# Performance work log

Measured on AMD Instinct MI355X. Metric: run time of the kernel, lower is better.

## Reference

```python
import jax, jax.numpy as jnp
import numpy as np

N_NODES = 50000
DIM_IN = 256
DIM_OUT = 256
N_EDGES = 1600000


def setup_inputs() -> dict:
    key = jax.random.key(0)
    k1, k2, k3, k4, k5 = jax.random.split(key, 5)
    feature = jax.random.normal(k1, (N_NODES, DIM_IN), dtype=jnp.float32)
    src = jax.random.randint(k2, (N_EDGES,), 0, N_NODES, dtype=jnp.int32)
    dst = jax.random.randint(k3, (N_EDGES,), 0, N_NODES, dtype=jnp.int32)
    # Linear(dim_in, dim_out) params
    bound = 1.0 / np.sqrt(DIM_IN)
    W = jax.random.uniform(k4, (DIM_OUT, DIM_IN), dtype=jnp.float32, minval=-bound, maxval=bound)
    b = jax.random.uniform(k5, (DIM_OUT,), dtype=jnp.float32, minval=-bound, maxval=bound)
    return {"feature": feature, "src": src, "dst": dst, "W": W, "b": b}


def reference(feature, src, dst, W, b):
    # copy_u: gather source features per edge; mean-reduce per destination node.
    msg_sum = jax.ops.segment_sum(feature[src], dst, num_segments=N_NODES)  # [N, Din]
    deg = jax.ops.segment_sum(jnp.ones((src.shape[0],), feature.dtype), dst,
                              num_segments=N_NODES)  # [N]
    mean = msg_sum / jnp.maximum(deg, 1.0)[:, None]
    # DGL update_all only overwrites 'h' for nodes that received messages;
    # isolated (in-degree 0) nodes keep their original feature.
    h = jnp.where((deg > 0)[:, None], mean, feature)
    # apply_nodes: Linear on all nodes
    return h @ W.T + b
```

## Files before the change

kernel.cpp:

```cpp
#include <hip/hip_runtime.h>
#include <hip/hip_bf16.h>

#define N_NODES 50000
#define NPAD 50016
#define DUMMY 50000
#define DIM 256
#define N_EDGES 1600000
#define NBUK 196
#define CAP 10240
#define CHUNK_E 4096
#define NBLK ((N_EDGES + CHUNK_E - 1) / CHUNK_E)
#define GEMM_BLKS ((N_NODES + 63) / 64)
#define NCHUNK 8
#define AGG_BPC 782
#define NGROUP (N_NODES / 16)
#define LROW 72

typedef float f32x4 __attribute__((ext_vector_type(4)));
typedef __bf16 bf16x8 __attribute__((ext_vector_type(8)));
typedef __bf16 bf16x4 __attribute__((ext_vector_type(4)));
typedef unsigned long long u64;
typedef unsigned int u32;
typedef unsigned short u16;

__global__ __launch_bounds__(256) void setup_k(const float* __restrict__ W,
                                               __bf16* __restrict__ Wbf,
                                               int* __restrict__ bcur,
                                               __bf16* __restrict__ Yc) {
    int i = blockIdx.x * 256 + threadIdx.x;
    Wbf[i] = (__bf16)W[i];
    if (i < NBUK) bcur[i] = i * CAP;
    if (i < NCHUNK * (NPAD - N_NODES) * 32) {
        int c = i >> 9;
        int rem = i & 511;
        Yc[(size_t)c * NPAD * 32 + (size_t)(N_NODES + (rem >> 5)) * 32 + (rem & 31)] = (__bf16)0.0f;
    }
}

__global__ __launch_bounds__(256) void fused_k(const float* __restrict__ feat,
                                               const __bf16* __restrict__ Wbf,
                                               __bf16* __restrict__ Yc,
                                               const int* __restrict__ src,
                                               const int* __restrict__ dst,
                                               int* __restrict__ bcur,
                                               unsigned int* __restrict__ staged) {
    __shared__ __bf16 lw[256 * LROW];
    __shared__ int lh[NBUK];
    __shared__ int lbase[NBUK];

    if (blockIdx.x < GEMM_BLKS) {
        const int wid  = threadIdx.x >> 6;
        const int lane = threadIdx.x & 63;
        const int row0 = blockIdx.x * 64 + wid * 16;
        const int mrow = lane & 15;
        const int kgrp = lane >> 4;

        int arow = row0 + mrow;
        int arow_c = arow < N_NODES ? arow : (N_NODES - 1);
        const float* aptr = feat + (size_t)arow_c * DIM + kgrp * 8;

        const int t = threadIdx.x;
        const int srow = t >> 3;
        const int scb  = (t & 7) * 8;

        f32x4 acc[16];
#pragma unroll
        for (int i = 0; i < 16; ++i) acc[i] = (f32x4)0.0f;

        for (int p = 0; p < 4; ++p) {
            f32x4 ar0 = *(const f32x4*)(aptr + (p * 2) * 32);
            f32x4 ar1 = *(const f32x4*)(aptr + (p * 2) * 32 + 4);
            f32x4 ar2 = *(const f32x4*)(aptr + (p * 2 + 1) * 32);
            f32x4 ar3 = *(const f32x4*)(aptr + (p * 2 + 1) * 32 + 4);

            if (p) __syncthreads();
#pragma unroll
            for (int i = 0; i < 8; ++i) {
                int row = srow + i * 32;
                uint4 v = *(const uint4*)(Wbf + (size_t)row * DIM + p * 64 + scb);
                *(uint4*)(lw + row * LROW + scb) = v;
            }
            __syncthreads();

            bf16x8 af0, af1;
            af0[0] = (__bf16)ar0[0]; af0[1] = (__bf16)ar0[1];
            af0[2] = (__bf16)ar0[2]; af0[3] = (__bf16)ar0[3];
            af0[4] = (__bf16)ar1[0]; af0[5] = (__bf16)ar1[1];
            af0[6] = (__bf16)ar1[2]; af0[7] = (__bf16)ar1[3];
            af1[0] = (__bf16)ar2[0]; af1[1] = (__bf16)ar2[1];
            af1[2] = (__bf16)ar2[2]; af1[3] = (__bf16)ar2[3];
            af1[4] = (__bf16)ar3[0]; af1[5] = (__bf16)ar3[1];
            af1[6] = (__bf16)ar3[2]; af1[7] = (__bf16)ar3[3];

#pragma unroll
            for (int nt = 0; nt < 16; ++nt) {
                const __bf16* lp = lw + (nt * 16 + mrow) * LROW + kgrp * 8;
                bf16x8 wf0 = *(const bf16x8*)(lp);
                bf16x8 wf1 = *(const bf16x8*)(lp + 32);
                acc[nt] = __builtin_amdgcn_mfma_f32_16x16x32_bf16(wf0, af0, acc[nt], 0, 0, 0);
                acc[nt] = __builtin_amdgcn_mfma_f32_16x16x32_bf16(wf1, af1, acc[nt], 0, 0, 0);
            }
        }

        const int node = row0 + mrow;
        if (node < N_NODES) {
#pragma unroll
            for (int nt = 0; nt < 16; ++nt) {
                int oc0 = nt * 16 + kgrp * 4;
                bf16x4 pv;
                pv[0] = (__bf16)acc[nt][0];
                pv[1] = (__bf16)acc[nt][1];
                pv[2] = (__bf16)acc[nt][2];
                pv[3] = (__bf16)acc[nt][3];
                __bf16* yp = Yc + (size_t)(oc0 >> 5) * NPAD * 32
                                + (size_t)node * 32 + (oc0 & 31);
                *(bf16x4*)yp = pv;
            }
        }
    } else {
        int pb = blockIdx.x - GEMM_BLKS;
        for (int i = threadIdx.x; i < NBUK; i += 256) lh[i] = 0;
        __syncthreads();
        int base = pb * CHUNK_E;
        int end = base + CHUNK_E; if (end > N_EDGES) end = N_EDGES;
        for (int e = base + threadIdx.x; e < end; e += 256)
            atomicAdd(&lh[dst[e] >> 8], 1);
        __syncthreads();
        for (int i = threadIdx.x; i < NBUK; i += 256) {
            int c = lh[i];
            lbase[i] = c ? atomicAdd(&bcur[i], c) : 0;
            lh[i] = 0;
        }
        __syncthreads();
        for (int e = base + threadIdx.x; e < end; e += 256) {
            int d = dst[e];
            int s = src[e];
            int b = d >> 8;
            int p = atomicAdd(&lh[b], 1);
            staged[lbase[b] + p] = (unsigned int)s | ((unsigned int)(d & 255) << 16);
        }
    }
}

__global__ __launch_bounds__(256) void finalize_k(const unsigned int* __restrict__ staged,
                                                  const int* __restrict__ bcur,
                                                  int* __restrict__ offs,
                                                  u16* __restrict__ deg16,
                                                  u16* __restrict__ edge16) {
    __shared__ int nh[256];
    __shared__ int nbase[256];
    __shared__ int sm[256];
    int t = threadIdx.x, b = blockIdx.x;
    int beg = b * CAP;
    int cnt = bcur[b] - beg;
    nh[t] = 0;
    __syncthreads();
    for (int i = t; i < cnt; i += 256)
        atomicAdd(&nh[staged[beg + i] >> 16], 1);
    __syncthreads();
    int v = nh[t];
    int v8 = (v + 7) & ~7;
    sm[t] = v8;
    __syncthreads();
    for (int off = 1; off < 256; off <<= 1) {
        int x = (t >= off) ? sm[t - off] : 0;
        __syncthreads();
        sm[t] += x;
        __syncthreads();
    }
    nbase[t] = sm[t] - v8;
    int node = (b << 8) + t;
    if (node < N_NODES) {
        offs[node]  = beg + nbase[t];
        deg16[node] = (u16)v;
    }
    for (int i = v; i < v8; ++i)
        edge16[beg + nbase[t] + i] = (u16)DUMMY;
    nh[t] = 0;
    __syncthreads();
    for (int i = t; i < cnt; i += 256) {
        unsigned int u = staged[beg + i];
        int dl = (int)(u >> 16);
        int p = atomicAdd(&nh[dl], 1);
        edge16[beg + nbase[dl] + p] = (u16)(u & 0xFFFFu);
    }
}

#define GQ(ev) (*(const uint4*)(Ybase + (size_t)((u32)(ev) & 0xffffu) * 32 + cl))
#define ACCQ(q) do { \
    a0 += __uint_as_float((q).x << 16); a1 += __uint_as_float((q).x); \
    a2 += __uint_as_float((q).y << 16); a3 += __uint_as_float((q).y); \
    a4 += __uint_as_float((q).z << 16); a5 += __uint_as_float((q).z); \
    a6 += __uint_as_float((q).w << 16); a7 += __uint_as_float((q).w); \
} while (0)

__global__ __launch_bounds__(256) void aggregate_k(const __bf16* __restrict__ Yc,
                                                   const int* __restrict__ offs,
                                                   const u16* __restrict__ deg16,
                                                   const u16* __restrict__ edge16,
                                                   const float* __restrict__ bias,
                                                   float* __restrict__ out) {
    const int chunk = blockIdx.x & 7;
    const int bic   = blockIdx.x >> 3;
    const int wid   = threadIdx.x >> 6;
    const int lane  = threadIdx.x & 63;
    const int seg   = lane >> 2;
    const int cl    = (lane & 3) * 8;

    const int g = bic * 4 + wid;
    if (g >= NGROUP) return;
    const int node = g * 16 + seg;

    const __bf16* Ybase = Yc + (size_t)chunk * NPAD * 32;
    const float* bp = bias + chunk * 32 + cl;
    const f32x4 bv0 = *(const f32x4*)bp;
    const f32x4 bv1 = *(const f32x4*)(bp + 4);

    const int beg = offs[node];
    const int dg  = (int)deg16[node];

    float a0 = 0.f, a1 = 0.f, a2 = 0.f, a3 = 0.f;
    float a4 = 0.f, a5 = 0.f, a6 = 0.f, a7 = 0.f;

    f32x4 r0, r1;
    if (dg > 0) {
        const int nb8 = (dg + 7) >> 3;
        const int npair = nb8 >> 1;
        const int odd = nb8 & 1;
        int j = beg;
        u64 eA = *(const u64*)(edge16 + j);
        u64 eB = *(const u64*)(edge16 + j + 4);
        u64 eC = *(const u64*)(edge16 + j + 8);
        u64 eD = *(const u64*)(edge16 + j + 12);
        for (int p = 0; p < npair; ++p) {
            u64 nA = *(const u64*)(edge16 + j + 16);
            u64 nB = *(const u64*)(edge16 + j + 20);
            u64 nC = *(const u64*)(edge16 + j + 24);
            u64 nD = *(const u64*)(edge16 + j + 28);
            uint4 q0 = GQ(eA);       uint4 q1 = GQ(eA >> 16);
            uint4 q2 = GQ(eA >> 32); uint4 q3 = GQ(eA >> 48);
            uint4 q4 = GQ(eB);       uint4 q5 = GQ(eB >> 16);
            uint4 q6 = GQ(eB >> 32); uint4 q7 = GQ(eB >> 48);
            uint4 q8 = GQ(eC);       uint4 q9 = GQ(eC >> 16);
            uint4 qa = GQ(eC >> 32); uint4 qb = GQ(eC >> 48);
            uint4 qc = GQ(eD);       uint4 qd = GQ(eD >> 16);
            uint4 qe = GQ(eD >> 32); uint4 qf = GQ(eD >> 48);
            ACCQ(q0); ACCQ(q1); ACCQ(q2); ACCQ(q3);
            ACCQ(q4); ACCQ(q5); ACCQ(q6); ACCQ(q7);
            ACCQ(q8); ACCQ(q9); ACCQ(qa); ACCQ(qb);
            ACCQ(qc); ACCQ(qd); ACCQ(qe); ACCQ(qf);
            j += 16;
            eA = nA; eB = nB; eC = nC; eD = nD;
        }
        if (odd) {
            uint4 q0 = GQ(eA);       uint4 q1 = GQ(eA >> 16);
            uint4 q2 = GQ(eA >> 32); uint4 q3 = GQ(eA >> 48);
            uint4 q4 = GQ(eB);       uint4 q5 = GQ(eB >> 16);
            uint4 q6 = GQ(eB >> 32); uint4 q7 = GQ(eB >> 48);
            ACCQ(q0); ACCQ(q1); ACCQ(q2); ACCQ(q3);
            ACCQ(q4); ACCQ(q5); ACCQ(q6); ACCQ(q7);
        }
        float inv = 1.0f / (float)dg;
        r0[0] = a0 * inv + bv0[0];
        r0[1] = a1 * inv + bv0[1];
        r0[2] = a2 * inv + bv0[2];
        r0[3] = a3 * inv + bv0[3];
        r1[0] = a4 * inv + bv1[0];
        r1[1] = a5 * inv + bv1[1];
        r1[2] = a6 * inv + bv1[2];
        r1[3] = a7 * inv + bv1[3];
    } else {
        uint4 q = *(const uint4*)(Ybase + (size_t)node * 32 + cl);
        r0[0] = __uint_as_float(q.x << 16) + bv0[0];
        r0[1] = __uint_as_float(q.x & 0xffff0000u) + bv0[1];
        r0[2] = __uint_as_float(q.y << 16) + bv0[2];
        r0[3] = __uint_as_float(q.y & 0xffff0000u) + bv0[3];
        r1[0] = __uint_as_float(q.z << 16) + bv1[0];
        r1[1] = __uint_as_float(q.z & 0xffff0000u) + bv1[1];
        r1[2] = __uint_as_float(q.w << 16) + bv1[2];
        r1[3] = __uint_as_float(q.w & 0xffff0000u) + bv1[3];
    }
    float* op = out + (size_t)node * DIM + chunk * 32 + cl;
    *(f32x4*)op = r0;
    *(f32x4*)(op + 4) = r1;
}

static inline size_t align64(size_t x) { return (x + 63) & ~(size_t)63; }

extern "C" void kernel_launch(void* const* d_in, const int* in_sizes, int n_in,
                              void* d_out, int out_size, void* d_ws, size_t ws_size,
                              hipStream_t stream) {
    const float* feature = (const float*)d_in[0];
    const int*   src     = (const int*)d_in[1];
    const int*   dst     = (const int*)d_in[2];
    const float* W       = (const float*)d_in[3];
    const float* b       = (const float*)d_in[4];
    float* out = (float*)d_out;

    char* ws = (char*)d_ws;
    __bf16* Yc  = (__bf16*)ws;               ws += align64((size_t)NCHUNK * NPAD * 32 * 2);
    __bf16* Wbf = (__bf16*)ws;               ws += align64((size_t)DIM * DIM * 2);
    int* offs     = (int*)ws;                ws += align64((size_t)N_NODES * 4);
    u16* deg16    = (u16*)ws;                ws += align64((size_t)N_NODES * 2);
    int* bcur     = (int*)ws;                ws += align64((size_t)NBUK * 4);
    unsigned int* staged = (unsigned int*)ws; ws += align64((size_t)NBUK * CAP * 4);
    u16* edge16   = (u16*)ws;                ws += align64((size_t)NBUK * CAP * 2 + 128);

    setup_k<<<(DIM * DIM) / 256, 256, 0, stream>>>(W, Wbf, bcur, Yc);
    fused_k<<<GEMM_BLKS + NBLK, 256, 0, stream>>>(feature, Wbf, Yc, src, dst, bcur, staged);
    finalize_k<<<NBUK, 256, 0, stream>>>(staged, bcur, offs, deg16, edge16);
    aggregate_k<<<NCHUNK * AGG_BPC, 256, 0, stream>>>(Yc, offs, deg16, edge16, b, out);
}
```

Baseline: 143.2 us.

## Restage pipeline: bucket edges with W convert, run GEMM alongside CSR finalize

Reorganises the kernel schedule. Edge bucketing now runs with the W-to-bf16 conversion and Y padding zeroing in a new prep kernel. The GEMM then runs in the same launch as the per-bucket CSR finalize, which saves one kernel launch and lets the finalize work overlap the GEMM. bcur now counts from zero (cleared by a memset) and the bucket base is added separately. A sched_barrier is also placed in the aggregate loop so all gathers issue before the accumulation.

```diff
diff --git a/kernel.cpp b/kernel.cpp
--- a/kernel.cpp
+++ b/kernel.cpp
@@ -23,30 +23,66 @@
 typedef unsigned int u32;
 typedef unsigned short u16;
 
-__global__ __launch_bounds__(256) void setup_k(const float* __restrict__ W,
-                                               __bf16* __restrict__ Wbf,
-                                               int* __restrict__ bcur,
-                                               __bf16* __restrict__ Yc) {
-    int i = blockIdx.x * 256 + threadIdx.x;
-    Wbf[i] = (__bf16)W[i];
-    if (i < NBUK) bcur[i] = i * CAP;
-    if (i < NCHUNK * (NPAD - N_NODES) * 32) {
-        int c = i >> 9;
-        int rem = i & 511;
-        Yc[(size_t)c * NPAD * 32 + (size_t)(N_NODES + (rem >> 5)) * 32 + (rem & 31)] = (__bf16)0.0f;
+__global__ __launch_bounds__(256) void prep_k(const float* __restrict__ W,
+                                              __bf16* __restrict__ Wbf,
+                                              __bf16* __restrict__ Yc,
+                                              const int* __restrict__ src,
+                                              const int* __restrict__ dst,
+                                              int* __restrict__ bcur,
+                                              unsigned int* __restrict__ staged) {
+    __shared__ int lh[NBUK];
+    __shared__ int lbase[NBUK];
+
+    if (blockIdx.x < NBLK) {
+        int pb = blockIdx.x;
+        for (int i = threadIdx.x; i < NBUK; i += 256) lh[i] = 0;
+        __syncthreads();
+        int base = pb * CHUNK_E;
+        int end = base + CHUNK_E; if (end > N_EDGES) end = N_EDGES;
+        for (int e = base + threadIdx.x; e < end; e += 256)
+            atomicAdd(&lh[dst[e] >> 8], 1);
+        __syncthreads();
+        for (int i = threadIdx.x; i < NBUK; i += 256) {
+            int c = lh[i];
+            lbase[i] = c ? (atomicAdd(&bcur[i], c) + i * CAP) : 0;
+            lh[i] = 0;
+        }
+        __syncthreads();
+        for (int e = base + threadIdx.x; e < end; e += 256) {
+            int d = dst[e];
+            int s = src[e];
+            int b = d >> 8;
+            int p = atomicAdd(&lh[b], 1);
+            staged[lbase[b] + p] = (unsigned int)s | ((unsigned int)(d & 255) << 16);
+        }
+    } else {
+        int p = blockIdx.x - NBLK;
+        if (p < 256) {
+            int i = p * 256 + threadIdx.x;
+            Wbf[i] = (__bf16)W[i];
+        } else {
+            for (int i = threadIdx.x; i < NCHUNK * 16 * 32; i += 256) {
+                int c = i >> 9;
+                int rem = i & 511;
+                Yc[(size_t)c * NPAD * 32 + (size_t)(N_NODES + (rem >> 5)) * 32 + (rem & 31)]
+                    = (__bf16)0.0f;
+            }
+        }
     }
 }
 
-__global__ __launch_bounds__(256) void fused_k(const float* __restrict__ feat,
-                                               const __bf16* __restrict__ Wbf,
-                                               __bf16* __restrict__ Yc,
-                                               const int* __restrict__ src,
-                                               const int* __restrict__ dst,
-                                               int* __restrict__ bcur,
-                                               unsigned int* __restrict__ staged) {
+__global__ __launch_bounds__(256) void gemmfin_k(const float* __restrict__ feat,
+                                                 const __bf16* __restrict__ Wbf,
+                                                 __bf16* __restrict__ Yc,
+                                                 const unsigned int* __restrict__ staged,
+                                                 const int* __restrict__ bcur,
+                                                 int* __restrict__ offs,
+                                                 u16* __restrict__ deg16,
+                                                 u16* __restrict__ edge16) {
     __shared__ __bf16 lw[256 * LROW];
-    __shared__ int lh[NBUK];
-    __shared__ int lbase[NBUK];
+    __shared__ int nh[256];
+    __shared__ int nbase[256];
+    __shared__ int sm[256];
 
     if (blockIdx.x < GEMM_BLKS) {
         const int wid  = threadIdx.x >> 6;
@@ -118,71 +154,40 @@
             }
         }
     } else {
-        int pb = blockIdx.x - GEMM_BLKS;
-        for (int i = threadIdx.x; i < NBUK; i += 256) lh[i] = 0;
-        __syncthreads();
-        int base = pb * CHUNK_E;
-        int end = base + CHUNK_E; if (end > N_EDGES) end = N_EDGES;
-        for (int e = base + threadIdx.x; e < end; e += 256)
-            atomicAdd(&lh[dst[e] >> 8], 1);
-        __syncthreads();
-        for (int i = threadIdx.x; i < NBUK; i += 256) {
-            int c = lh[i];
-            lbase[i] = c ? atomicAdd(&bcur[i], c) : 0;
-            lh[i] = 0;
-        }
-        __syncthreads();
-        for (int e = base + threadIdx.x; e < end; e += 256) {
-            int d = dst[e];
-            int s = src[e];
-            int b = d >> 8;
-            int p = atomicAdd(&lh[b], 1);
-            staged[lbase[b] + p] = (unsigned int)s | ((unsigned int)(d & 255) << 16);
-        }
-    }
-}
-
-__global__ __launch_bounds__(256) void finalize_k(const unsigned int* __restrict__ staged,
-                                                  const int* __restrict__ bcur,
-                                                  int* __restrict__ offs,
-                                                  u16* __restrict__ deg16,
-                                                  u16* __restrict__ edge16) {
-    __shared__ int nh[256];
-    __shared__ int nbase[256];
-    __shared__ int sm[256];
-    int t = threadIdx.x, b = blockIdx.x;
-    int beg = b * CAP;
-    int cnt = bcur[b] - beg;
-    nh[t] = 0;
-    __syncthreads();
-    for (int i = t; i < cnt; i += 256)
-        atomicAdd(&nh[staged[beg + i] >> 16], 1);
-    __syncthreads();
-    int v = nh[t];
-    int v8 = (v + 7) & ~7;
-    sm[t] = v8;
-    __syncthreads();
-    for (int off = 1; off < 256; off <<= 1) {
-        int x = (t >= off) ? sm[t - off] : 0;
-        __syncthreads();
-        sm[t] += x;
-        __syncthreads();
-    }
-    nbase[t] = sm[t] - v8;
-    int node = (b << 8) + t;
-    if (node < N_NODES) {
-        offs[node]  = beg + nbase[t];
-        deg16[node] = (u16)v;
-    }
-    for (int i = v; i < v8; ++i)
-        edge16[beg + nbase[t] + i] = (u16)DUMMY;
-    nh[t] = 0;
-    __syncthreads();
-    for (int i = t; i < cnt; i += 256) {
-        unsigned int u = staged[beg + i];
-        int dl = (int)(u >> 16);
-        int p = atomicAdd(&nh[dl], 1);
-        edge16[beg + nbase[dl] + p] = (u16)(u & 0xFFFFu);
+        int t = threadIdx.x, b = blockIdx.x - GEMM_BLKS;
+        int beg = b * CAP;
+        int cnt = bcur[b];
+        nh[t] = 0;
+        __syncthreads();
+        for (int i = t; i < cnt; i += 256)
+            atomicAdd(&nh[staged[beg + i] >> 16], 1);
+        __syncthreads();
+        int v = nh[t];
+        int v8 = (v + 7) & ~7;
+        sm[t] = v8;
+        __syncthreads();
+        for (int off = 1; off < 256; off <<= 1) {
+            int x = (t >= off) ? sm[t - off] : 0;
+            __syncthreads();
+            sm[t] += x;
+            __syncthreads();
+        }
+        nbase[t] = sm[t] - v8;
+        int node = (b << 8) + t;
+        if (node < N_NODES) {
+            offs[node]  = beg + nbase[t];
+            deg16[node] = (u16)v;
+        }
+        for (int i = v; i < v8; ++i)
+            edge16[beg + nbase[t] + i] = (u16)DUMMY;
+        nh[t] = 0;
+        __syncthreads();
+        for (int i = t; i < cnt; i += 256) {
+            unsigned int u = staged[beg + i];
+            int dl = (int)(u >> 16);
+            int p = atomicAdd(&nh[dl], 1);
+            edge16[beg + nbase[dl] + p] = (u16)(u & 0xFFFFu);
+        }
     }
 }
 
@@ -245,6 +250,7 @@
             uint4 qa = GQ(eC >> 32); uint4 qb = GQ(eC >> 48);
             uint4 qc = GQ(eD);       uint4 qd = GQ(eD >> 16);
             uint4 qe = GQ(eD >> 32); uint4 qf = GQ(eD >> 48);
+            __builtin_amdgcn_sched_barrier(0);
             ACCQ(q0); ACCQ(q1); ACCQ(q2); ACCQ(q3);
             ACCQ(q4); ACCQ(q5); ACCQ(q6); ACCQ(q7);
             ACCQ(q8); ACCQ(q9); ACCQ(qa); ACCQ(qb);
@@ -306,8 +312,9 @@
     unsigned int* staged = (unsigned int*)ws; ws += align64((size_t)NBUK * CAP * 4);
     u16* edge16   = (u16*)ws;                ws += align64((size_t)NBUK * CAP * 2 + 128);
 
-    setup_k<<<(DIM * DIM) / 256, 256, 0, stream>>>(W, Wbf, bcur, Yc);
-    fused_k<<<GEMM_BLKS + NBLK, 256, 0, stream>>>(feature, Wbf, Yc, src, dst, bcur, staged);
-    finalize_k<<<NBUK, 256, 0, stream>>>(staged, bcur, offs, deg16, edge16);
+    hipMemsetAsync(bcur, 0, (size_t)NBUK * 4, stream);
+    prep_k<<<NBLK + 257, 256, 0, stream>>>(W, Wbf, Yc, src, dst, bcur, staged);
+    gemmfin_k<<<GEMM_BLKS + NBUK, 256, 0, stream>>>(feature, Wbf, Yc, staged, bcur,
+                                                    offs, deg16, edge16);
     aggregate_k<<<NCHUNK * AGG_BPC, 256, 0, stream>>>(Yc, offs, deg16, edge16, b, out);
 }
```

Result: no change. 144.7 us (+1.1%).
